# Performance work log

Hardware: AMD Instinct MI355X
Metric: run time of the kernel (lower is better)

## Reference

```python
import jax, jax.numpy as jnp
import numpy as np

B, N, M = 2, 4096, 4096
QUERY_DIM = 1024
CONTEXT_DIM = 1024
HEADS = 16
DIM_HEAD = 64
INNER = HEADS * DIM_HEAD


def setup_inputs() -> dict:
    key = jax.random.key(0)
    ks = jax.random.split(key, 7)
    s = 0.02
    return {
        "x": jax.random.normal(ks[0], (B, N, QUERY_DIM), dtype=jnp.float32),
        "context": jax.random.normal(ks[1], (B, M, CONTEXT_DIM), dtype=jnp.float32),
        "Wq": jax.random.normal(ks[2], (QUERY_DIM, INNER), dtype=jnp.float32) * s,
        "Wk": jax.random.normal(ks[3], (CONTEXT_DIM, INNER), dtype=jnp.float32) * s,
        "Wv": jax.random.normal(ks[4], (CONTEXT_DIM, INNER), dtype=jnp.float32) * s,
        "Wo": jax.random.normal(ks[5], (INNER, QUERY_DIM), dtype=jnp.float32) * s,
        "bo": jnp.zeros((QUERY_DIM,), dtype=jnp.float32),
    }


def reference(x, context, Wq, Wk, Wv, Wo, bo):
    scale = DIM_HEAD ** -0.5
    # projections, then split heads: b n (h d) -> b h n d
    q = (x @ Wq).reshape(B, N, HEADS, DIM_HEAD).transpose(0, 2, 1, 3)
    k = (context @ Wk).reshape(B, M, HEADS, DIM_HEAD).transpose(0, 2, 1, 3)
    v = (context @ Wv).reshape(B, M, HEADS, DIM_HEAD).transpose(0, 2, 1, 3)
    attn = jnp.einsum('bhnd,bhmd->bhnm', q, k) * scale  # [B,H,N,M]
    attn = jax.nn.softmax(attn, axis=-1)
    out = jnp.einsum('bhnm,bhmd->bhnd', attn, v)
    out = out.transpose(0, 2, 1, 3).reshape(B, N, INNER)  # b h n d -> b n (h d)
    return out @ Wo + bo  # dropout(p=0) is identity
```

## Files before the change

kernel.cpp:

```cpp
#include <hip/hip_runtime.h>

using f16    = _Float16;
using f16x2  = __attribute__((ext_vector_type(2))) _Float16;
using f16x4  = __attribute__((ext_vector_type(4))) _Float16;
using f16x8  = __attribute__((ext_vector_type(8))) _Float16;
using h16x2  = __attribute__((ext_vector_type(2))) __fp16;
using f32x4  = __attribute__((ext_vector_type(4))) float;
using f32x16 = __attribute__((ext_vector_type(16))) float;
using u32    = unsigned int;
using u32x4  = __attribute__((ext_vector_type(4))) u32;

#define DI __device__ __forceinline__

DI f16x4 pack4(float a, float b, float c, float d) {
  f16x2 lo = __builtin_bit_cast(f16x2, __builtin_amdgcn_cvt_pkrtz(a, b));
  f16x2 hi = __builtin_bit_cast(f16x2, __builtin_amdgcn_cvt_pkrtz(c, d));
  f16x4 r; r[0] = lo[0]; r[1] = lo[1]; r[2] = hi[0]; r[3] = hi[1];
  return r;
}

DI u32 pk32(float a, float b) {
  return __builtin_bit_cast(u32, __builtin_amdgcn_cvt_pkrtz(a, b));
}

DI float dot1(u32 wrd, float acc) {
#if __has_builtin(__builtin_amdgcn_fdot2)
  h16x2 one; one[0] = (__fp16)1.f; one[1] = (__fp16)1.f;
  return __builtin_amdgcn_fdot2(__builtin_bit_cast(h16x2, wrd), one, acc, false);
#else
  f16x2 p = __builtin_bit_cast(f16x2, wrd);
  return acc + (float)p[0] + (float)p[1];
#endif
}

DI void gll16(const void* g, void* l) {
  __builtin_amdgcn_global_load_lds((const __attribute__((address_space(1))) u32*)g,
                                   (__attribute__((address_space(3))) u32*)l, 16, 0, 0);
}

DI f16x8 ldfrag(const void* base, int row, int u4) {
  int phys = u4 ^ (row & 7);
  return *(const f16x8*)((const char*)base + row * 128 + phys * 16);
}

DI f32x4 mfma16(f16x8 a, f16x8 b, f32x4 c) {
  return __builtin_amdgcn_mfma_f32_16x16x32_f16(a, b, c, 0, 0, 0);
}
DI f32x16 mfma32(f16x8 a, f16x8 b, f32x16 c) {
  return __builtin_amdgcn_mfma_f32_32x32x16_f16(a, b, c, 0, 0, 0);
}

__global__ void k_cvt2(const float* __restrict__ x, const float* __restrict__ ctx,
                       f16* __restrict__ dst, int n4) {
  int z = blockIdx.y;
  const float* s = z ? ctx : x;
  f16* d = dst + (size_t)z * 8192 * 1024;
  int i = blockIdx.x * blockDim.x + threadIdx.x;
  if (i < n4) {
    float4 v = ((const float4*)s)[i];
    ((f16x4*)d)[i] = pack4(v.x, v.y, v.z, v.w);
  }
}

__global__ void k_wt4(const float* __restrict__ Wq, const float* __restrict__ Wk,
                      const float* __restrict__ Wv, const float* __restrict__ Wo,
                      f16* __restrict__ WTb) {
  int z = blockIdx.z;
  const float* W = z == 0 ? Wq : z == 1 ? Wk : z == 2 ? Wv : Wo;
  f16* WT = WTb + (size_t)z * 1024 * 1024;
  __shared__ float tile[64][65];
  int k0 = blockIdx.y * 64, n0 = blockIdx.x * 64;
  int t = threadIdx.x;
#pragma unroll
  for (int p = 0; p < 4; ++p) {
    int r = p * 16 + (t >> 4);
    int c = (t & 15) * 4;
    float4 v = *(const float4*)&W[(size_t)(k0 + r) * 1024 + n0 + c];
    tile[r][c] = v.x; tile[r][c + 1] = v.y; tile[r][c + 2] = v.z; tile[r][c + 3] = v.w;
  }
  __syncthreads();
#pragma unroll
  for (int p = 0; p < 4; ++p) {
    int n = p * 16 + (t >> 4);
    int k = (t & 15) * 4;
    *(f16x4*)&WT[(size_t)(n0 + n) * 1024 + k0 + k] =
        pack4(tile[k][n], tile[k + 1][n], tile[k + 2][n], tile[k + 3][n]);
  }
}

template <int EPI>
__global__ __launch_bounds__(256) void k_gemm(const f16* __restrict__ A, const f16* __restrict__ Bt,
                                              void* __restrict__ Cp, const float* __restrict__ bias) {
  __shared__ __align__(16) char smem[65536];
  f16* sA = (f16*)smem;
  f16* sB = (f16*)(smem + 32768);
  const int tid = threadIdx.x, w = tid >> 6, lane = tid & 63;
  const int g = lane >> 4, l15 = lane & 15, l7 = lane & 7, l8 = lane >> 3;
  const int m0 = blockIdx.x * 128, n0 = blockIdx.y * 128;
  const int wm = w >> 1, wn = w & 1;
  const int uswz = l7 ^ l8;

  auto stage = [&](int kt, int bufi) {
    int kb = kt * 128;
#pragma unroll
    for (int q = 0; q < 4; ++q) {
      int row = w * 32 + q * 8 + l8;
      gll16((const char*)A + (size_t)(m0 + row) * 2048 + kb + uswz * 16,
            (char*)sA + bufi * 16384 + (w * 32 + q * 8) * 128);
      gll16((const char*)Bt + (size_t)(n0 + row) * 2048 + kb + uswz * 16,
            (char*)sB + bufi * 16384 + (w * 32 + q * 8) * 128);
    }
  };

  f32x4 acc[4][4] = {};
  stage(0, 0);
  for (int kt = 0; kt < 16; ++kt) {
    asm volatile("s_waitcnt vmcnt(0)" ::: "memory");
    __syncthreads();
    if (kt + 1 < 16) stage(kt + 1, (kt + 1) & 1);
    const f16* aL = (const f16*)((const char*)sA + (kt & 1) * 16384);
    const f16* bL = (const f16*)((const char*)sB + (kt & 1) * 16384);
#pragma unroll
    for (int kc = 0; kc < 2; ++kc) {
      f16x8 af[4], bf[4];
#pragma unroll
      for (int mi = 0; mi < 4; ++mi) af[mi] = ldfrag(aL, wm * 64 + mi * 16 + l15, kc * 4 + g);
#pragma unroll
      for (int ni = 0; ni < 4; ++ni) bf[ni] = ldfrag(bL, wn * 64 + ni * 16 + l15, kc * 4 + g);
#pragma unroll
      for (int mi = 0; mi < 4; ++mi)
#pragma unroll
        for (int ni = 0; ni < 4; ++ni) acc[mi][ni] = mfma16(af[mi], bf[ni], acc[mi][ni]);
    }
  }

  if (EPI == 2) {
    float* C = (float*)Cp;
    float bv[4];
#pragma unroll
    for (int ni = 0; ni < 4; ++ni) bv[ni] = bias[n0 + wn * 64 + ni * 16 + l15];
#pragma unroll
    for (int mi = 0; mi < 4; ++mi)
#pragma unroll
      for (int ni = 0; ni < 4; ++ni) {
        int col = n0 + wn * 64 + ni * 16 + l15;
#pragma unroll
        for (int i = 0; i < 4; ++i) {
          int row = m0 + wm * 64 + mi * 16 + g * 4 + i;
          C[(size_t)row * 1024 + col] = acc[mi][ni][i] + bv[ni];
        }
      }
    return;
  }

  __syncthreads();
  f16* Ct = (f16*)smem;
  if (EPI == 0 || EPI == 3) {
#pragma unroll
    for (int mi = 0; mi < 4; ++mi)
#pragma unroll
      for (int ni = 0; ni < 4; ++ni) {
        int col = wn * 64 + ni * 16 + l15;
#pragma unroll
        for (int i = 0; i < 4; ++i) Ct[(wm * 64 + mi * 16 + g * 4 + i) * 136 + col] = (f16)acc[mi][ni][i];
      }
    __syncthreads();
    if (EPI == 0) {
      f16* C = (f16*)Cp;
#pragma unroll
      for (int p = 0; p < 8; ++p) {
        int r = p * 16 + (tid >> 4), cu = tid & 15;
        f16x8 v = *(const f16x8*)((const char*)Ct + r * 272 + cu * 16);
        *(f16x8*)((char*)C + (size_t)(m0 + r) * 2048 + n0 * 2 + cu * 16) = v;
      }
    } else {
      int b = m0 >> 12, mmr = m0 & 4095;
#pragma unroll
      for (int p = 0; p < 8; ++p) {
        int r = p * 16 + (tid >> 4), cu = tid & 15;
        f16x8 v = *(const f16x8*)((const char*)Ct + r * 272 + cu * 16);
        int kvr = mmr + r;
        int h = (n0 >> 6) + (cu >> 3);
        size_t off = ((size_t)((b * 16 + h) * 64 + (kvr >> 6))) * 8192 + (cu & 7) * 1024 + (kvr & 63) * 16;
        *(f16x8*)((char*)Cp + off) = v;
      }
    }
  } else {
#pragma unroll
    for (int mi = 0; mi < 4; ++mi)
#pragma unroll
      for (int ni = 0; ni < 4; ++ni) {
        int n = wn * 64 + ni * 16 + l15;
        int mcol = wm * 64 + mi * 16 + g * 4;
        *(f16x4*)&Ct[n * 136 + mcol] =
            pack4(acc[mi][ni][0], acc[mi][ni][1], acc[mi][ni][2], acc[mi][ni][3]);
      }
    __syncthreads();
    int b = m0 >> 12, mm = m0 & 4095;
#pragma unroll
    for (int p = 0; p < 8; ++p) {
      int r = p * 16 + (tid >> 4), cu = tid & 15;
      f16x8 v = *(const f16x8*)((const char*)Ct + r * 272 + cu * 16);
      int h = (n0 + r) >> 6, d = (n0 + r) & 63;
      size_t off = ((size_t)((b * 16 + h) * 64 + (mm >> 6) + (cu >> 3))) * 8192 + (cu & 7) * 1024 + d * 16;
      *(f16x8*)((char*)Cp + off) = v;
    }
  }
}

__global__ __launch_bounds__(256, 2) void k_attn(const f16* __restrict__ Qh, const f16* __restrict__ Ks,
                                                 const f16* __restrict__ Vs, f16* __restrict__ Oh) {
  __shared__ __align__(16) char smem[32768];
  const int tid = threadIdx.x, w = tid >> 6, lane = tid & 63;
  const int hi = lane >> 5, c = lane & 31, l7 = lane & 7, l8 = lane >> 3;
  const int bid = blockIdx.x;
  const int bh = (bid & 7) * 4 + (bid >> 7);
  const int qc = (bid >> 3) & 15;
  const int b = bh >> 4, h = bh & 15;
  const int rowB = b * 4096;
  const int qrow0 = rowB + qc * 256 + w * 64;
  const size_t tb = (size_t)bh * 64 * 8192;

  const int offA0 = hi * 1024 + c * 16;
  const int offA1 = offA0 + 512;

  const f16 ce = (f16)0.18033688f;
  f16x8 bQ0[4], bQ1[4];
#pragma unroll
  for (int ks = 0; ks < 4; ++ks) {
    f16x8 r0 = *(const f16x8*)(Qh + (size_t)(qrow0 + c) * 1024 + h * 64 + ks * 16 + hi * 8);
    f16x8 r1 = *(const f16x8*)(Qh + (size_t)(qrow0 + 32 + c) * 1024 + h * 64 + ks * 16 + hi * 8);
#pragma unroll
    for (int e = 0; e < 8; ++e) { r0[e] *= ce; r1[e] *= ce; }
    bQ0[ks] = r0; bQ1[ks] = r1;
  }

  const f32x16 Z = {};
  f32x16 acc00 = {}, acc01 = {}, acc10 = {}, acc11 = {};
  float lrow0 = 0.f, lrow1 = 0.f;

  auto softpack = [&](f32x16 sA, f32x16 sB, f16x8* bp) -> float {
#pragma unroll
    for (int i = 0; i < 16; ++i) sA[i] = __builtin_amdgcn_exp2f(sA[i]);
#pragma unroll
    for (int i = 0; i < 16; ++i) sB[i] = __builtin_amdgcn_exp2f(sB[i]);
    u32 a[8], d[8];
#pragma unroll
    for (int i = 0; i < 8; ++i) a[i] = pk32(sA[2 * i], sA[2 * i + 1]);
#pragma unroll
    for (int i = 0; i < 8; ++i) d[i] = pk32(sB[2 * i], sB[2 * i + 1]);
    float s0 = 0.f, s1 = 0.f;
#pragma unroll
    for (int i = 0; i < 8; ++i) s0 = dot1(a[i], s0);
#pragma unroll
    for (int i = 0; i < 8; ++i) s1 = dot1(d[i], s1);
    {
      auto s02 = __builtin_amdgcn_permlane32_swap(a[0], a[2], false, false);
      auto s13 = __builtin_amdgcn_permlane32_swap(a[1], a[3], false, false);
      auto s46 = __builtin_amdgcn_permlane32_swap(a[4], a[6], false, false);
      auto s57 = __builtin_amdgcn_permlane32_swap(a[5], a[7], false, false);
      u32x4 w0 = {s02[0], s13[0], s02[1], s13[1]};
      u32x4 w1 = {s46[0], s57[0], s46[1], s57[1]};
      bp[0] = __builtin_bit_cast(f16x8, w0);
      bp[1] = __builtin_bit_cast(f16x8, w1);
    }
    {
      auto s02 = __builtin_amdgcn_permlane32_swap(d[0], d[2], false, false);
      auto s13 = __builtin_amdgcn_permlane32_swap(d[1], d[3], false, false);
      auto s46 = __builtin_amdgcn_permlane32_swap(d[4], d[6], false, false);
      auto s57 = __builtin_amdgcn_permlane32_swap(d[5], d[7], false, false);
      u32x4 w0 = {s02[0], s13[0], s02[1], s13[1]};
      u32x4 w1 = {s46[0], s57[0], s46[1], s57[1]};
      bp[2] = __builtin_bit_cast(f16x8, w0);
      bp[3] = __builtin_bit_cast(f16x8, w1);
    }
    return s0 + s1;
  };

#pragma unroll 1
  for (int t = 0; t < 64; ++t) {
    const char* pK = (const char*)Ks + tb + (size_t)t * 8192;
    const char* pV = (const char*)Vs + tb + (size_t)t * 8192;

    f16x8 kf[8], vf[8];
#pragma unroll
    for (int ks = 0; ks < 4; ++ks) {
      kf[ks * 2]     = *(const f16x8*)(pK + ks * 2048 + offA0);
      kf[ks * 2 + 1] = *(const f16x8*)(pK + ks * 2048 + offA1);
    }
#pragma unroll
    for (int ks = 0; ks < 4; ++ks) {
      vf[ks * 2]     = *(const f16x8*)(pV + ks * 2048 + offA0);
      vf[ks * 2 + 1] = *(const f16x8*)(pV + ks * 2048 + offA1);
    }

    __builtin_amdgcn_s_setprio(1);
    f32x16 st00 = mfma32(kf[0], bQ0[0], Z);
    f32x16 st01 = mfma32(kf[0], bQ1[0], Z);
    f32x16 st10 = mfma32(kf[1], bQ0[0], Z);
    f32x16 st11 = mfma32(kf[1], bQ1[0], Z);
#pragma unroll
    for (int ks = 1; ks < 4; ++ks) {
      st00 = mfma32(kf[ks * 2], bQ0[ks], st00);
      st01 = mfma32(kf[ks * 2], bQ1[ks], st01);
      st10 = mfma32(kf[ks * 2 + 1], bQ0[ks], st10);
      st11 = mfma32(kf[ks * 2 + 1], bQ1[ks], st11);
    }
    __builtin_amdgcn_s_setprio(0);

    f16x8 bpA[4], bpB[4];
    lrow0 += softpack(st00, st10, bpA);
    lrow1 += softpack(st01, st11, bpB);

    __builtin_amdgcn_s_setprio(1);
#pragma unroll
    for (int ks = 0; ks < 4; ++ks) {
      acc00 = mfma32(vf[ks * 2], bpA[ks], acc00);
      acc01 = mfma32(vf[ks * 2], bpB[ks], acc01);
      acc10 = mfma32(vf[ks * 2 + 1], bpA[ks], acc10);
      acc11 = mfma32(vf[ks * 2 + 1], bpB[ks], acc11);
    }
    __builtin_amdgcn_s_setprio(0);
  }

  float inv0, inv1;
  {
    auto r2 = __builtin_amdgcn_permlane32_swap(__builtin_bit_cast(u32, lrow0),
                                               __builtin_bit_cast(u32, lrow0), false, false);
    inv0 = 1.0f / (__builtin_bit_cast(float, r2[0]) + __builtin_bit_cast(float, r2[1]));
  }
  {
    auto r2 = __builtin_amdgcn_permlane32_swap(__builtin_bit_cast(u32, lrow1),
                                               __builtin_bit_cast(u32, lrow1), false, false);
    inv1 = 1.0f / (__builtin_bit_cast(float, r2[0]) + __builtin_bit_cast(float, r2[1]));
  }

  char* myO = (char*)smem + w * 8192;
#pragma unroll
  for (int rb = 0; rb < 2; ++rb) {
    float iv = rb ? inv1 : inv0;
    int r = rb * 32 + c;
#pragma unroll
    for (int dt = 0; dt < 2; ++dt) {
      const f32x16& A = rb ? (dt ? acc11 : acc01) : (dt ? acc10 : acc00);
#pragma unroll
      for (int q8 = 0; q8 < 4; ++q8) {
        f16x4 hv = pack4(A[q8 * 4] * iv, A[q8 * 4 + 1] * iv, A[q8 * 4 + 2] * iv, A[q8 * 4 + 3] * iv);
        int slot = dt * 4 + q8;
        *(f16x4*)(myO + r * 128 + ((slot ^ (r & 7)) * 16) + hi * 8) = hv;
      }
    }
  }
#pragma unroll
  for (int p = 0; p < 8; ++p) {
    int r = p * 8 + l8;
    f16x8 v = *(const f16x8*)(myO + r * 128 + ((l7 ^ (r & 7)) * 16));
    *(f16x8*)((char*)Oh + ((size_t)(qrow0 + r) * 1024 + h * 64) * 2 + l7 * 16) = v;
  }
}

extern "C" void kernel_launch(void* const* d_in, const int* in_sizes, int n_in,
                              void* d_out, int out_size, void* d_ws, size_t ws_size,
                              hipStream_t stream) {
  const float* x   = (const float*)d_in[0];
  const float* ctx = (const float*)d_in[1];
  const float* Wq  = (const float*)d_in[2];
  const float* Wk  = (const float*)d_in[3];
  const float* Wv  = (const float*)d_in[4];
  const float* Wo  = (const float*)d_in[5];
  const float* bo  = (const float*)d_in[6];
  float* out = (float*)d_out;

  const size_t NR = 8192, KD = 1024;
  if (ws_size < (size_t)(5 * NR * KD * 2 + 4 * KD * KD * 2)) return;

  char* ws = (char*)d_ws;
  f16* xh  = (f16*)ws;
  f16* ch  = xh + NR * KD;
  f16* WqT = ch + NR * KD;
  f16* WkT = WqT + KD * KD;
  f16* WvT = WkT + KD * KD;
  f16* WoT = WvT + KD * KD;
  f16* Qh  = WoT + KD * KD;
  f16* Ks  = Qh + NR * KD;
  f16* Vs  = Ks + NR * KD;
  f16* Oh  = xh;

  int n4 = (int)(NR * KD / 4);
  k_cvt2<<<dim3((n4 + 255) / 256, 2), dim3(256), 0, stream>>>(x, ctx, xh, n4);
  k_wt4<<<dim3(16, 16, 4), dim3(256), 0, stream>>>(Wq, Wk, Wv, Wo, WqT);

  dim3 gg(64, 8), gb(256);
  k_gemm<0><<<gg, gb, 0, stream>>>(xh, WqT, (void*)Qh, nullptr);
  k_gemm<3><<<gg, gb, 0, stream>>>(ch, WkT, (void*)Ks, nullptr);
  k_gemm<1><<<gg, gb, 0, stream>>>(ch, WvT, (void*)Vs, nullptr);

  k_attn<<<dim3(512), dim3(256), 0, stream>>>(Qh, Ks, Vs, Oh);

  k_gemm<2><<<gg, gb, 0, stream>>>(Oh, WoT, (void*)out, bo);
}
```

Measured before the change: 282.0 us.

## Prefetch next K/V fragments and interleave softmax halves with PV MFMAs

```diff
diff --git a/kernel.cpp b/kernel.cpp
--- a/kernel.cpp
+++ b/kernel.cpp
@@ -48,6 +48,27 @@
 }
 DI f32x16 mfma32(f16x8 a, f16x8 b, f32x16 c) {
   return __builtin_amdgcn_mfma_f32_32x32x16_f16(a, b, c, 0, 0, 0);
+}
+
+DI void softhalf(const f32x16& s, f16x8* bp2, float& lr) {
+  f32x16 e;
+#pragma unroll
+  for (int i = 0; i < 16; ++i) e[i] = __builtin_amdgcn_exp2f(s[i]);
+  u32 a[8];
+#pragma unroll
+  for (int i = 0; i < 8; ++i) a[i] = pk32(e[2 * i], e[2 * i + 1]);
+  float s0 = lr;
+#pragma unroll
+  for (int i = 0; i < 8; ++i) s0 = dot1(a[i], s0);
+  lr = s0;
+  auto s02 = __builtin_amdgcn_permlane32_swap(a[0], a[2], false, false);
+  auto s13 = __builtin_amdgcn_permlane32_swap(a[1], a[3], false, false);
+  auto s46 = __builtin_amdgcn_permlane32_swap(a[4], a[6], false, false);
+  auto s57 = __builtin_amdgcn_permlane32_swap(a[5], a[7], false, false);
+  u32x4 w0 = {s02[0], s13[0], s02[1], s13[1]};
+  u32x4 w1 = {s46[0], s57[0], s46[1], s57[1]};
+  bp2[0] = __builtin_bit_cast(f16x8, w0);
+  bp2[1] = __builtin_bit_cast(f16x8, w1);
 }
 
 __global__ void k_cvt2(const float* __restrict__ x, const float* __restrict__ ctx,
@@ -239,88 +260,86 @@
   f32x16 acc00 = {}, acc01 = {}, acc10 = {}, acc11 = {};
   float lrow0 = 0.f, lrow1 = 0.f;
 
-  auto softpack = [&](f32x16 sA, f32x16 sB, f16x8* bp) -> float {
-#pragma unroll
-    for (int i = 0; i < 16; ++i) sA[i] = __builtin_amdgcn_exp2f(sA[i]);
-#pragma unroll
-    for (int i = 0; i < 16; ++i) sB[i] = __builtin_amdgcn_exp2f(sB[i]);
-    u32 a[8], d[8];
-#pragma unroll
-    for (int i = 0; i < 8; ++i) a[i] = pk32(sA[2 * i], sA[2 * i + 1]);
-#pragma unroll
-    for (int i = 0; i < 8; ++i) d[i] = pk32(sB[2 * i], sB[2 * i + 1]);
-    float s0 = 0.f, s1 = 0.f;
-#pragma unroll
-    for (int i = 0; i < 8; ++i) s0 = dot1(a[i], s0);
-#pragma unroll
-    for (int i = 0; i < 8; ++i) s1 = dot1(d[i], s1);
-    {
-      auto s02 = __builtin_amdgcn_permlane32_swap(a[0], a[2], false, false);
-      auto s13 = __builtin_amdgcn_permlane32_swap(a[1], a[3], false, false);
-      auto s46 = __builtin_amdgcn_permlane32_swap(a[4], a[6], false, false);
-      auto s57 = __builtin_amdgcn_permlane32_swap(a[5], a[7], false, false);
-      u32x4 w0 = {s02[0], s13[0], s02[1], s13[1]};
-      u32x4 w1 = {s46[0], s57[0], s46[1], s57[1]};
-      bp[0] = __builtin_bit_cast(f16x8, w0);
-      bp[1] = __builtin_bit_cast(f16x8, w1);
-    }
-    {
-      auto s02 = __builtin_amdgcn_permlane32_swap(d[0], d[2], false, false);
-      auto s13 = __builtin_amdgcn_permlane32_swap(d[1], d[3], false, false);
-      auto s46 = __builtin_amdgcn_permlane32_swap(d[4], d[6], false, false);
-      auto s57 = __builtin_amdgcn_permlane32_swap(d[5], d[7], false, false);
-      u32x4 w0 = {s02[0], s13[0], s02[1], s13[1]};
-      u32x4 w1 = {s46[0], s57[0], s46[1], s57[1]};
-      bp[2] = __builtin_bit_cast(f16x8, w0);
-      bp[3] = __builtin_bit_cast(f16x8, w1);
-    }
-    return s0 + s1;
-  };
-
-#pragma unroll 1
-  for (int t = 0; t < 64; ++t) {
+  f16x8 kf[8], vf[8];
+  auto loadK = [&](int t) {
     const char* pK = (const char*)Ks + tb + (size_t)t * 8192;
-    const char* pV = (const char*)Vs + tb + (size_t)t * 8192;
-
-    f16x8 kf[8], vf[8];
 #pragma unroll
     for (int ks = 0; ks < 4; ++ks) {
       kf[ks * 2]     = *(const f16x8*)(pK + ks * 2048 + offA0);
       kf[ks * 2 + 1] = *(const f16x8*)(pK + ks * 2048 + offA1);
     }
+  };
+  auto loadV = [&](int t) {
+    const char* pV = (const char*)Vs + tb + (size_t)t * 8192;
 #pragma unroll
     for (int ks = 0; ks < 4; ++ks) {
       vf[ks * 2]     = *(const f16x8*)(pV + ks * 2048 + offA0);
       vf[ks * 2 + 1] = *(const f16x8*)(pV + ks * 2048 + offA1);
     }
+  };
+
+  loadK(0);
+  loadV(0);
+#pragma unroll 1
+  for (int t = 0; t < 64; ++t) {
+    int tn = (t + 1) & 63;
 
     __builtin_amdgcn_s_setprio(1);
     f32x16 st00 = mfma32(kf[0], bQ0[0], Z);
     f32x16 st01 = mfma32(kf[0], bQ1[0], Z);
-    f32x16 st10 = mfma32(kf[1], bQ0[0], Z);
-    f32x16 st11 = mfma32(kf[1], bQ1[0], Z);
 #pragma unroll
     for (int ks = 1; ks < 4; ++ks) {
       st00 = mfma32(kf[ks * 2], bQ0[ks], st00);
       st01 = mfma32(kf[ks * 2], bQ1[ks], st01);
+    }
+    f32x16 st10 = mfma32(kf[1], bQ0[0], Z);
+    f32x16 st11 = mfma32(kf[1], bQ1[0], Z);
+#pragma unroll
+    for (int ks = 1; ks < 4; ++ks) {
       st10 = mfma32(kf[ks * 2 + 1], bQ0[ks], st10);
       st11 = mfma32(kf[ks * 2 + 1], bQ1[ks], st11);
     }
     __builtin_amdgcn_s_setprio(0);
+    __builtin_amdgcn_sched_barrier(0);
+
+    loadK(tn);
+    __builtin_amdgcn_sched_barrier(0);
 
     f16x8 bpA[4], bpB[4];
-    lrow0 += softpack(st00, st10, bpA);
-    lrow1 += softpack(st01, st11, bpB);
+    softhalf(st00, &bpA[0], lrow0);
+    softhalf(st01, &bpB[0], lrow1);
+    __builtin_amdgcn_sched_barrier(0);
 
     __builtin_amdgcn_s_setprio(1);
-#pragma unroll
-    for (int ks = 0; ks < 4; ++ks) {
-      acc00 = mfma32(vf[ks * 2], bpA[ks], acc00);
-      acc01 = mfma32(vf[ks * 2], bpB[ks], acc01);
-      acc10 = mfma32(vf[ks * 2 + 1], bpA[ks], acc10);
-      acc11 = mfma32(vf[ks * 2 + 1], bpB[ks], acc11);
-    }
+    acc00 = mfma32(vf[0], bpA[0], acc00);
+    acc01 = mfma32(vf[0], bpB[0], acc01);
+    acc10 = mfma32(vf[1], bpA[0], acc10);
+    acc11 = mfma32(vf[1], bpB[0], acc11);
+    acc00 = mfma32(vf[2], bpA[1], acc00);
+    acc01 = mfma32(vf[2], bpB[1], acc01);
+    acc10 = mfma32(vf[3], bpA[1], acc10);
+    acc11 = mfma32(vf[3], bpB[1], acc11);
     __builtin_amdgcn_s_setprio(0);
+    __builtin_amdgcn_sched_barrier(0);
+
+    softhalf(st10, &bpA[2], lrow0);
+    softhalf(st11, &bpB[2], lrow1);
+    __builtin_amdgcn_sched_barrier(0);
+
+    __builtin_amdgcn_s_setprio(1);
+    acc00 = mfma32(vf[4], bpA[2], acc00);
+    acc01 = mfma32(vf[4], bpB[2], acc01);
+    acc10 = mfma32(vf[5], bpA[2], acc10);
+    acc11 = mfma32(vf[5], bpB[2], acc11);
+    acc00 = mfma32(vf[6], bpA[3], acc00);
+    acc01 = mfma32(vf[6], bpB[3], acc01);
+    acc10 = mfma32(vf[7], bpA[3], acc10);
+    acc11 = mfma32(vf[7], bpB[3], acc11);
+    __builtin_amdgcn_s_setprio(0);
+    __builtin_amdgcn_sched_barrier(0);
+
+    loadV(tn);
+    __builtin_amdgcn_sched_barrier(0);
   }
 
   float inv0, inv1;
```

Measured after the change: 281.7 us. Within noise of the previous version (-0.1%).

## Stage K/V tiles through double-buffered LDS with async global_load_lds

Applied to the files above, without the earlier changes.

```diff
diff --git a/kernel.cpp b/kernel.cpp
--- a/kernel.cpp
+++ b/kernel.cpp
@@ -43,11 +43,36 @@
   return *(const f16x8*)((const char*)base + row * 128 + phys * 16);
 }
 
+DI f16x8 ldsc(const void* base, int row, int slot) {
+  return *(const f16x8*)((const char*)base + slot * 1024 + row * 16);
+}
+
 DI f32x4 mfma16(f16x8 a, f16x8 b, f32x4 c) {
   return __builtin_amdgcn_mfma_f32_16x16x32_f16(a, b, c, 0, 0, 0);
 }
 DI f32x16 mfma32(f16x8 a, f16x8 b, f32x16 c) {
   return __builtin_amdgcn_mfma_f32_32x32x16_f16(a, b, c, 0, 0, 0);
+}
+
+DI void softhalf(const f32x16& s, f16x8* bp2, float& lr) {
+  f32x16 e;
+#pragma unroll
+  for (int i = 0; i < 16; ++i) e[i] = __builtin_amdgcn_exp2f(s[i]);
+  u32 a[8];
+#pragma unroll
+  for (int i = 0; i < 8; ++i) a[i] = pk32(e[2 * i], e[2 * i + 1]);
+  float s0 = lr;
+#pragma unroll
+  for (int i = 0; i < 8; ++i) s0 = dot1(a[i], s0);
+  lr = s0;
+  auto s02 = __builtin_amdgcn_permlane32_swap(a[0], a[2], false, false);
+  auto s13 = __builtin_amdgcn_permlane32_swap(a[1], a[3], false, false);
+  auto s46 = __builtin_amdgcn_permlane32_swap(a[4], a[6], false, false);
+  auto s57 = __builtin_amdgcn_permlane32_swap(a[5], a[7], false, false);
+  u32x4 w0 = {s02[0], s13[0], s02[1], s13[1]};
+  u32x4 w1 = {s46[0], s57[0], s46[1], s57[1]};
+  bp2[0] = __builtin_bit_cast(f16x8, w0);
+  bp2[1] = __builtin_bit_cast(f16x8, w1);
 }
 
 __global__ void k_cvt2(const float* __restrict__ x, const float* __restrict__ ctx,
@@ -221,9 +246,6 @@
   const int qrow0 = rowB + qc * 256 + w * 64;
   const size_t tb = (size_t)bh * 64 * 8192;
 
-  const int offA0 = hi * 1024 + c * 16;
-  const int offA1 = offA0 + 512;
-
   const f16 ce = (f16)0.18033688f;
   f16x8 bQ0[4], bQ1[4];
 #pragma unroll
@@ -239,59 +261,31 @@
   f32x16 acc00 = {}, acc01 = {}, acc10 = {}, acc11 = {};
   float lrow0 = 0.f, lrow1 = 0.f;
 
-  auto softpack = [&](f32x16 sA, f32x16 sB, f16x8* bp) -> float {
-#pragma unroll
-    for (int i = 0; i < 16; ++i) sA[i] = __builtin_amdgcn_exp2f(sA[i]);
-#pragma unroll
-    for (int i = 0; i < 16; ++i) sB[i] = __builtin_amdgcn_exp2f(sB[i]);
-    u32 a[8], d[8];
-#pragma unroll
-    for (int i = 0; i < 8; ++i) a[i] = pk32(sA[2 * i], sA[2 * i + 1]);
-#pragma unroll
-    for (int i = 0; i < 8; ++i) d[i] = pk32(sB[2 * i], sB[2 * i + 1]);
-    float s0 = 0.f, s1 = 0.f;
-#pragma unroll
-    for (int i = 0; i < 8; ++i) s0 = dot1(a[i], s0);
-#pragma unroll
-    for (int i = 0; i < 8; ++i) s1 = dot1(d[i], s1);
-    {
-      auto s02 = __builtin_amdgcn_permlane32_swap(a[0], a[2], false, false);
-      auto s13 = __builtin_amdgcn_permlane32_swap(a[1], a[3], false, false);
-      auto s46 = __builtin_amdgcn_permlane32_swap(a[4], a[6], false, false);
-      auto s57 = __builtin_amdgcn_permlane32_swap(a[5], a[7], false, false);
-      u32x4 w0 = {s02[0], s13[0], s02[1], s13[1]};
-      u32x4 w1 = {s46[0], s57[0], s46[1], s57[1]};
-      bp[0] = __builtin_bit_cast(f16x8, w0);
-      bp[1] = __builtin_bit_cast(f16x8, w1);
-    }
-    {
-      auto s02 = __builtin_amdgcn_permlane32_swap(d[0], d[2], false, false);
-      auto s13 = __builtin_amdgcn_permlane32_swap(d[1], d[3], false, false);
-      auto s46 = __builtin_amdgcn_permlane32_swap(d[4], d[6], false, false);
-      auto s57 = __builtin_amdgcn_permlane32_swap(d[5], d[7], false, false);
-      u32x4 w0 = {s02[0], s13[0], s02[1], s13[1]};
-      u32x4 w1 = {s46[0], s57[0], s46[1], s57[1]};
-      bp[2] = __builtin_bit_cast(f16x8, w0);
-      bp[3] = __builtin_bit_cast(f16x8, w1);
-    }
-    return s0 + s1;
+  auto stage = [&](int t, int bufi) {
+    const char* gK = (const char*)Ks + tb + (size_t)t * 8192 + w * 2048 + lane * 16;
+    const char* gV = (const char*)Vs + tb + (size_t)t * 8192 + w * 2048 + lane * 16;
+    char* dK = (char*)smem + bufi * 8192 + w * 2048;
+    char* dV = (char*)smem + 16384 + bufi * 8192 + w * 2048;
+    gll16(gK, dK);
+    gll16(gK + 1024, dK + 1024);
+    gll16(gV, dV);
+    gll16(gV + 1024, dV + 1024);
   };
 
+  stage(0, 0);
 #pragma unroll 1
   for (int t = 0; t < 64; ++t) {
-    const char* pK = (const char*)Ks + tb + (size_t)t * 8192;
-    const char* pV = (const char*)Vs + tb + (size_t)t * 8192;
-
-    f16x8 kf[8], vf[8];
+    asm volatile("s_waitcnt vmcnt(0)" ::: "memory");
+    __syncthreads();
+    if (t + 1 < 64) stage(t + 1, (t + 1) & 1);
+    const char* Kl = (const char*)smem + (t & 1) * 8192;
+    const char* Vl = (const char*)smem + 16384 + (t & 1) * 8192;
+
+    f16x8 kf[8];
 #pragma unroll
     for (int ks = 0; ks < 4; ++ks) {
-      kf[ks * 2]     = *(const f16x8*)(pK + ks * 2048 + offA0);
-      kf[ks * 2 + 1] = *(const f16x8*)(pK + ks * 2048 + offA1);
-    }
-#pragma unroll
-    for (int ks = 0; ks < 4; ++ks) {
-      vf[ks * 2]     = *(const f16x8*)(pV + ks * 2048 + offA0);
-      vf[ks * 2 + 1] = *(const f16x8*)(pV + ks * 2048 + offA1);
+      kf[ks * 2]     = ldsc(Kl, c, ks * 2 + hi);
+      kf[ks * 2 + 1] = ldsc(Kl, 32 + c, ks * 2 + hi);
     }
 
     __builtin_amdgcn_s_setprio(1);
@@ -308,9 +302,18 @@
     }
     __builtin_amdgcn_s_setprio(0);
 
+    f16x8 vf[8];
+#pragma unroll
+    for (int ks = 0; ks < 4; ++ks) {
+      vf[ks * 2]     = ldsc(Vl, c, ks * 2 + hi);
+      vf[ks * 2 + 1] = ldsc(Vl, 32 + c, ks * 2 + hi);
+    }
+
     f16x8 bpA[4], bpB[4];
-    lrow0 += softpack(st00, st10, bpA);
-    lrow1 += softpack(st01, st11, bpB);
+    softhalf(st00, &bpA[0], lrow0);
+    softhalf(st01, &bpB[0], lrow1);
+    softhalf(st10, &bpA[2], lrow0);
+    softhalf(st11, &bpB[2], lrow1);
 
     __builtin_amdgcn_s_setprio(1);
 #pragma unroll
@@ -335,6 +338,7 @@
     inv1 = 1.0f / (__builtin_bit_cast(float, r2[0]) + __builtin_bit_cast(float, r2[1]));
   }
 
+  __syncthreads();
   char* myO = (char*)smem + w * 8192;
 #pragma unroll
   for (int rb = 0; rb < 2; ++rb) {
```

New measurement: 269.0 us. 1.05x faster.
